# Optimization experiments

Hardware: AMD Instinct MI355X
Metric: run time of the kernel (lower is better)

The kernel has to match this reference:

```python
import jax, jax.numpy as jnp
import numpy as np

B, N, C, NUM_WINDOWS = 8, 40962, 128, 162  # ico-6 vertices, ico-2 centers


def _make_window_ids():
    # Mirrors __init__: assign each high-res vertex to nearest center (Voronoi on sphere).
    rng = np.random.default_rng(0)
    v = rng.normal(size=(N, 3)).astype(np.float32)
    v /= np.linalg.norm(v, axis=1, keepdims=True)
    c = rng.normal(size=(NUM_WINDOWS, 3)).astype(np.float32)
    c /= np.linalg.norm(c, axis=1, keepdims=True)
    d = np.linalg.norm(v[:, None, :] - c[None, :, :], axis=-1)  # [N, 162] cdist
    return np.argmin(d, axis=1).astype(np.int32)


def setup_inputs() -> dict:
    key = jax.random.key(0)
    wid = _make_window_ids()
    counts = np.bincount(wid, minlength=NUM_WINDOWS)
    max_win_size = int(counts.max())  # static: window_ids is a fixed buffer
    x = jax.random.normal(key, (B, N, C), dtype=jnp.float32)
    return {
        "x": x,
        "window_ids": jnp.asarray(wid),
        "num_windows": NUM_WINDOWS,
        "max_win_size": max_win_size,
    }


def reference(x, window_ids, num_windows, max_win_size):
    Bx, Nx, Cx = x.shape
    # Sort vertices by window id (stable keeps within-window order deterministic).
    order = jnp.argsort(window_ids, stable=True)          # [N]
    x_sorted = x[:, order, :]                             # [B, N, C]
    counts = jnp.bincount(window_ids, length=num_windows) # [W]
    offsets = jnp.cumsum(counts) - counts                 # exclusive prefix sum [W]
    w_sorted = window_ids[order]                          # [N] window of each sorted vertex
    pos = jnp.arange(Nx) - offsets[w_sorted]              # slot within its window
    # Single fused scatter replaces the per-window Python loop + slice copies.
    x_windows = jnp.zeros((Bx, num_windows, max_win_size, Cx), dtype=x.dtype)
    x_windows = x_windows.at[:, w_sorted, pos, :].set(x_sorted)
    windows = x_windows.reshape(Bx * num_windows, max_win_size, Cx)
    return windows, order, counts
```

## Files before the change

kernel.cpp:

```cpp
#include <hip/hip_runtime.h>

typedef float f32x4 __attribute__((ext_vector_type(4)));

#define NW_MAX 192
#define CHUNK  1024
#define GCAP   48
#define RPB    64

__global__ __launch_bounds__(1024) void k_hist(
        const int* __restrict__ wid, int N, int NW, int* __restrict__ hist) {
    __shared__ int lh[NW_MAX];
    const int t = threadIdx.x;
    if (t < NW) lh[t] = 0;
    __syncthreads();
    const int i = blockIdx.x * CHUNK + t;
    if (i < N) atomicAdd(&lh[wid[i]], 1);
    __syncthreads();
    if (t < NW) hist[blockIdx.x * NW + t] = lh[t];
}

__global__ __launch_bounds__(1024) void k_order(
        const int* __restrict__ wid, int N, int NW, int G,
        const int* __restrict__ hist,
        int* __restrict__ offsets,
        int* __restrict__ sorted_src,
        float* __restrict__ order_f,
        float* __restrict__ counts_f) {
    __shared__ int lh[GCAP * NW_MAX];
    __shared__ int lw[CHUNK];
    __shared__ int cw[16 * NW_MAX];
    __shared__ int cnt_s[NW_MAX];
    __shared__ int lbase[NW_MAX];
    __shared__ int sc[256];

    const int t = threadIdx.x;
    const int g = blockIdx.x;
    const int total = G * NW;

    for (int idx = t; idx < total; idx += 1024) lh[idx] = hist[idx];
    for (int idx = t; idx < 16 * NW; idx += 1024) cw[idx] = 0;

    const int i = g * CHUNK + t;
    const int w = (i < N) ? wid[i] : -1;
    lw[t] = w;
    const int wv = t >> 6;
    __syncthreads();

    if (w >= 0) atomicAdd(&cw[wv * NW + w], 1);

    if (t < NW) {
        int s = 0;
        for (int gg = 0; gg < G; ++gg) s += lh[gg * NW + t];
        cnt_s[t] = s;
    }
    __syncthreads();

    if (t < 256) sc[t] = (t < NW) ? cnt_s[t] : 0;
    __syncthreads();
    for (int d = 1; d < 256; d <<= 1) {
        int v = 0;
        if (t < 256 && t >= d) v = sc[t - d];
        __syncthreads();
        if (t < 256) sc[t] += v;
        __syncthreads();
    }

    if (t < NW) {
        const int offw = (t == 0) ? 0 : sc[t - 1];
        int b = offw;
        for (int gg = 0; gg < g; ++gg) b += lh[gg * NW + t];
        lbase[t] = b;
        if (g == 0) {
            offsets[t] = offw;
            counts_f[t] = (float)cnt_s[t];
            if (t == 0) offsets[NW] = sc[NW - 1];
        }
    }
    __syncthreads();

    if (i < N) {
        int cr = 0;
        #pragma unroll
        for (int wv2 = 0; wv2 < 16; ++wv2)
            if (wv2 < wv) cr += cw[wv2 * NW + w];
        const int lane = t & 63;
        const int wb = t & ~63;
        int r = 0;
        #pragma unroll
        for (int j = 0; j < 63; ++j)
            if (j < lane && lw[wb + j] == w) ++r;
        const int p = lbase[w] + cr + r;
        order_f[p] = (float)i;
        sorted_src[p] = i;
    }
}

__global__ __launch_bounds__(256) void k_gather(
                         const f32x4* __restrict__ x,
                         const int* __restrict__ sorted_src,
                         const int* __restrict__ offsets,
                         int N, int NW, int MWS, int bpw,
                         f32x4* __restrict__ out) {
    const int w  = blockIdx.x / bpw;
    const int s0 = (blockIdx.x - w * bpw) * RPB;
    const int b  = blockIdx.y;
    const int t  = threadIdx.x;
    const int rl = t >> 5;
    const int c4 = t & 31;

    const int off = offsets[w];
    const int cnt = offsets[w + 1] - off;

    const long long xb = (long long)b * N;
    const long long ob = ((long long)b * NW + w) * MWS;

    int srcs[RPB / 8];
    #pragma unroll
    for (int k = 0; k < RPB / 8; ++k) {
        const int s = s0 + k * 8 + rl;
        srcs[k] = (s < cnt) ? sorted_src[off + s] : -1;
    }

    f32x4 v[RPB / 8];
    #pragma unroll
    for (int k = 0; k < RPB / 8; ++k) {
        const int sc = (srcs[k] >= 0) ? srcs[k] : 0;
        v[k] = x[(xb + sc) * 32 + c4];
    }

    #pragma unroll
    for (int k = 0; k < RPB / 8; ++k) {
        const int s = s0 + k * 8 + rl;
        if (s < MWS) {
            const f32x4 z = {0.f, 0.f, 0.f, 0.f};
            const f32x4 o = (srcs[k] >= 0) ? v[k] : z;
            __builtin_nontemporal_store(o, &out[(ob + s) * 32 + c4]);
        }
    }
}

extern "C" void kernel_launch(void* const* d_in, const int* in_sizes, int n_in,
                              void* d_out, int out_size, void* d_ws, size_t ws_size,
                              hipStream_t stream) {
    const float* x   = (const float*)d_in[0];
    const int*   wid = (const int*)d_in[1];

    const int N  = in_sizes[1];
    const int C  = 128;
    const int NW = 162;
    const int B  = (int)((long long)in_sizes[0] / ((long long)N * C));

    const long long win_elems = (long long)out_size - N - NW;
    const int MWS = (int)(win_elems / ((long long)B * NW * C));

    const int G = (N + CHUNK - 1) / CHUNK;

    int* hist       = (int*)d_ws;
    int* offsets    = hist + (size_t)G * NW;
    int* sorted_src = offsets + (NW + 1);

    float* out_f    = (float*)d_out;
    float* order_f  = out_f + win_elems;
    float* counts_f = order_f + N;

    const int bpw = (MWS + RPB - 1) / RPB;

    k_hist  <<<G, CHUNK, 0, stream>>>(wid, N, NW, hist);
    k_order <<<G, CHUNK, 0, stream>>>(wid, N, NW, G, hist, offsets,
                                      sorted_src, order_f, counts_f);
    k_gather<<<dim3(NW * bpw, B), 256, 0, stream>>>((const f32x4*)x, sorted_src,
                                                    offsets, N, NW, MWS, bpw,
                                                    (f32x4*)out_f);
}
```

Measured before the change: 102.5 us.

## Replace window gather with input-ordered scatter plus separate padding-zero blocks

The order kernel now records each vertex's slot within its window instead of a sorted source index. The copy kernel reads x contiguously in input order and scatters each row to its window slot. A separate group of blocks writes zeros only to padding rows. This trades random reads for random row writes and drops the nontemporal stores. Padding rows are no longer written as part of the main stream, which cuts work spent on empty slots.

```diff
diff --git a/kernel.cpp b/kernel.cpp
--- a/kernel.cpp
+++ b/kernel.cpp
@@ -5,7 +5,6 @@
 #define NW_MAX 192
 #define CHUNK  1024
 #define GCAP   48
-#define RPB    64
 
 __global__ __launch_bounds__(1024) void k_hist(
         const int* __restrict__ wid, int N, int NW, int* __restrict__ hist) {
@@ -23,7 +22,7 @@
         const int* __restrict__ wid, int N, int NW, int G,
         const int* __restrict__ hist,
         int* __restrict__ offsets,
-        int* __restrict__ sorted_src,
+        int* __restrict__ pos_i,
         float* __restrict__ order_f,
         float* __restrict__ counts_f) {
     __shared__ int lh[GCAP * NW_MAX];
@@ -31,6 +30,7 @@
     __shared__ int cw[16 * NW_MAX];
     __shared__ int cnt_s[NW_MAX];
     __shared__ int lbase[NW_MAX];
+    __shared__ int loff[NW_MAX];
     __shared__ int sc[256];
 
     const int t = threadIdx.x;
@@ -67,6 +67,7 @@
 
     if (t < NW) {
         const int offw = (t == 0) ? 0 : sc[t - 1];
+        loff[t] = offw;
         int b = offw;
         for (int gg = 0; gg < g; ++gg) b += lh[gg * NW + t];
         lbase[t] = b;
@@ -91,50 +92,64 @@
             if (j < lane && lw[wb + j] == w) ++r;
         const int p = lbase[w] + cr + r;
         order_f[p] = (float)i;
-        sorted_src[p] = i;
+        pos_i[i] = p - loff[w];
     }
 }
 
-__global__ __launch_bounds__(256) void k_gather(
-                         const f32x4* __restrict__ x,
-                         const int* __restrict__ sorted_src,
-                         const int* __restrict__ offsets,
-                         int N, int NW, int MWS, int bpw,
-                         f32x4* __restrict__ out) {
-    const int w  = blockIdx.x / bpw;
-    const int s0 = (blockIdx.x - w * bpw) * RPB;
-    const int b  = blockIdx.y;
-    const int t  = threadIdx.x;
-    const int rl = t >> 5;
-    const int c4 = t & 31;
+__global__ __launch_bounds__(256) void k_scatter(
+        const f32x4* __restrict__ x,
+        const int* __restrict__ wid,
+        const int* __restrict__ pos_i,
+        const int* __restrict__ offsets,
+        int N, int NW, int MWS, int DB, int S16,
+        f32x4* __restrict__ out) {
+    const int b = blockIdx.y;
+    const int t = threadIdx.x;
+    const long long ob = (long long)b * NW * MWS;
 
-    const int off = offsets[w];
-    const int cnt = offsets[w + 1] - off;
+    if ((int)blockIdx.x < DB) {
+        const int rl = t >> 5;
+        const int c4 = t & 31;
+        const int i0 = blockIdx.x * 32;
+        const long long xb = (long long)b * N;
 
-    const long long xb = (long long)b * N;
-    const long long ob = ((long long)b * NW + w) * MWS;
-
-    int srcs[RPB / 8];
-    #pragma unroll
-    for (int k = 0; k < RPB / 8; ++k) {
-        const int s = s0 + k * 8 + rl;
-        srcs[k] = (s < cnt) ? sorted_src[off + s] : -1;
-    }
-
-    f32x4 v[RPB / 8];
-    #pragma unroll
-    for (int k = 0; k < RPB / 8; ++k) {
-        const int sc = (srcs[k] >= 0) ? srcs[k] : 0;
-        v[k] = x[(xb + sc) * 32 + c4];
-    }
-
-    #pragma unroll
-    for (int k = 0; k < RPB / 8; ++k) {
-        const int s = s0 + k * 8 + rl;
-        if (s < MWS) {
-            const f32x4 z = {0.f, 0.f, 0.f, 0.f};
-            const f32x4 o = (srcs[k] >= 0) ? v[k] : z;
-            __builtin_nontemporal_store(o, &out[(ob + s) * 32 + c4]);
+        int wk[4], sk[4];
+        #pragma unroll
+        for (int k = 0; k < 4; ++k) {
+            const int i = i0 + k * 8 + rl;
+            wk[k] = (i < N) ? wid[i] : -1;
+            sk[k] = (i < N) ? pos_i[i] : 0;
+        }
+        f32x4 v[4];
+        #pragma unroll
+        for (int k = 0; k < 4; ++k) {
+            const int i = i0 + k * 8 + rl;
+            const int ic = (i < N) ? i : 0;
+            v[k] = x[(xb + ic) * 32 + c4];
+        }
+        #pragma unroll
+        for (int k = 0; k < 4; ++k) {
+            if (wk[k] >= 0)
+                out[(ob + (long long)wk[k] * MWS + sk[k]) * 32 + c4] = v[k];
+        }
+    } else {
+        const int e  = t >> 5;
+        const int c4 = t & 31;
+        const int ntup = NW * S16;
+        const int stride = gridDim.x - DB;
+        const f32x4 z = {0.f, 0.f, 0.f, 0.f};
+        for (int tup = blockIdx.x - DB; tup < ntup; tup += stride) {
+            const int w  = tup / S16;
+            const int s0 = (tup - w * S16) * 16;
+            const int cnt = offsets[w + 1] - offsets[w];
+            if (s0 + 16 <= cnt) continue;
+            const long long rb = ob + (long long)w * MWS;
+            #pragma unroll
+            for (int r = 0; r < 2; ++r) {
+                const int s = s0 + e * 2 + r;
+                if (s >= MWS || s < cnt) continue;
+                out[(rb + s) * 32 + c4] = z;
+            }
         }
     }
 }
@@ -155,20 +170,23 @@
 
     const int G = (N + CHUNK - 1) / CHUNK;
 
-    int* hist       = (int*)d_ws;
-    int* offsets    = hist + (size_t)G * NW;
-    int* sorted_src = offsets + (NW + 1);
+    int* hist    = (int*)d_ws;
+    int* offsets = hist + (size_t)G * NW;
+    int* pos_i   = offsets + (NW + 1);
 
     float* out_f    = (float*)d_out;
     float* order_f  = out_f + win_elems;
     float* counts_f = order_f + N;
 
-    const int bpw = (MWS + RPB - 1) / RPB;
+    const int DB   = (N + 31) / 32;
+    const int PADB = 256;
+    const int S16  = (MWS + 15) / 16;
 
-    k_hist  <<<G, CHUNK, 0, stream>>>(wid, N, NW, hist);
-    k_order <<<G, CHUNK, 0, stream>>>(wid, N, NW, G, hist, offsets,
-                                      sorted_src, order_f, counts_f);
-    k_gather<<<dim3(NW * bpw, B), 256, 0, stream>>>((const f32x4*)x, sorted_src,
-                                                    offsets, N, NW, MWS, bpw,
-                                                    (f32x4*)out_f);
+    k_hist   <<<G, CHUNK, 0, stream>>>(wid, N, NW, hist);
+    k_order  <<<G, CHUNK, 0, stream>>>(wid, N, NW, G, hist, offsets,
+                                       pos_i, order_f, counts_f);
+    k_scatter<<<dim3(DB + PADB, B), 256, 0, stream>>>((const f32x4*)x, wid,
+                                                      pos_i, offsets,
+                                                      N, NW, MWS, DB, S16,
+                                                      (f32x4*)out_f);
 }
```

Result: slower. 139.6 us (+36.2%).
